# Optimization experiments

Measured on AMD Instinct MI355X. Metric: run time of the kernel, lower is better.

The kernel has to match this reference:

```python
import jax, jax.numpy as jnp
import numpy as np
import math

DIM_IN, DIM_CTX, DIM_KEY, DIM_VAL = 2048, 512, 128, 128
N, T, H, W = 8, 16, 32, 32
NBOX = 512


def setup_inputs() -> dict:
    key = jax.random.key(0)
    ks = jax.random.split(key, 10)
    rois = jax.random.normal(ks[0], (NBOX, DIM_IN), dtype=jnp.float32)
    context = jax.random.normal(ks[1], (N, DIM_CTX, T, H, W), dtype=jnp.float32)
    batch_idx = jnp.sort(jax.random.randint(ks[2], (NBOX,), 0, N))
    s = 0.02
    W_proj = jax.random.normal(ks[3], (DIM_KEY, DIM_IN), dtype=jnp.float32) * s
    b_proj = jnp.zeros((DIM_KEY,), dtype=jnp.float32)
    W_keys = jax.random.normal(ks[4], (DIM_KEY, DIM_CTX), dtype=jnp.float32) * s
    b_keys = jnp.zeros((DIM_KEY,), dtype=jnp.float32)
    W_vals = jax.random.normal(ks[5], (DIM_VAL, DIM_CTX), dtype=jnp.float32) * s
    b_vals = jnp.zeros((DIM_VAL,), dtype=jnp.float32)
    return {"rois": rois, "context": context, "batch_idx": batch_idx,
            "W_proj": W_proj, "b_proj": b_proj,
            "W_keys": W_keys, "b_keys": b_keys,
            "W_vals": W_vals, "b_vals": b_vals}


def reference(rois, context, batch_idx, W_proj, b_proj, W_keys, b_keys, W_vals, b_vals):
    n, c, t, h, w = context.shape
    s = t * h * w
    dk = W_keys.shape[0]
    # ROI query projection: [Nb, dk]
    q = rois @ W_proj.T + b_proj
    # 1x1x1 Conv3d == per-voxel linear over channels
    ctx_flat = context.reshape(n, c, s)                       # [N, C, S]
    keys = jnp.einsum('kc,ncs->nks', W_keys, ctx_flat) + b_keys[None, :, None]  # [N, dk, S]
    vals = jnp.einsum('vc,ncs->nsv', W_vals, ctx_flat) + b_vals[None, None, :]  # [N, S, dv]
    # Per-box gather of its clip's keys/vals, fused cross-attention
    qk = jnp.einsum('bk,bks->bs', q, keys[batch_idx]) / math.sqrt(dk)  # [Nb, S]
    coeff = jax.nn.softmax(qk, axis=-1)
    ctx_out = jnp.einsum('bs,bsv->bv', coeff, vals[batch_idx])         # [Nb, dv]
    attn = coeff.reshape(-1, t, h, w) * 255.0
    return ctx_out, attn
```

## Files before the change

### kernel.cpp

```cpp
#include <hip/hip_runtime.h>
#include <hip/hip_bf16.h>
#include <math.h>

#define DIM_IN  2048
#define DIM_CTX 512
#define DIM_KEY 128
#define DIM_VAL 128
#define NCLIP   8
#define S_TOT   16384
#define NBOX    512
#define MAXB    96

typedef __attribute__((ext_vector_type(8))) short short8_t;
typedef __attribute__((ext_vector_type(4))) float f32x4;

__device__ inline unsigned short f2bf(float x) {
    union { float f; unsigned int u; } v; v.f = x;
    unsigned int r = v.u + 0x7FFFu + ((v.u >> 16) & 1u);
    return (unsigned short)(r >> 16);
}
__device__ inline float bf2f(unsigned short h) {
    union { unsigned int u; float f; } v; v.u = ((unsigned int)h) << 16;
    return v.f;
}

__global__ __launch_bounds__(256) void k0_init(const int* __restrict__ batch_idx,
                                               int* __restrict__ ranges,
                                               float* __restrict__ cctx) {
    int idx = blockIdx.x * blockDim.x + threadIdx.x;
    for (int i = idx; i < NBOX * DIM_CTX; i += gridDim.x * blockDim.x)
        cctx[i] = 0.0f;
    if (blockIdx.x == 0) {
        __shared__ int s_start[NCLIP], s_end[NCLIP];
        if (threadIdx.x < NCLIP) { s_start[threadIdx.x] = NBOX; s_end[threadIdx.x] = 0; }
        __syncthreads();
        for (int i = threadIdx.x; i < NBOX; i += blockDim.x) {
            int b = batch_idx[i];
            atomicMin(&s_start[b], i);
            atomicMax(&s_end[b], i + 1);
        }
        __syncthreads();
        if (threadIdx.x < NCLIP) {
            ranges[threadIdx.x]         = s_start[threadIdx.x];
            ranges[NCLIP + threadIdx.x] = s_end[threadIdx.x];
        }
    }
}

__global__ __launch_bounds__(128) void k1a_q(const float* __restrict__ rois,
                                             const float* __restrict__ W_proj,
                                             const float* __restrict__ b_proj,
                                             float* __restrict__ q) {
    __shared__ float s_roi[4 * DIM_IN];
    int b0 = blockIdx.x * 4;
    const float4* src = (const float4*)(rois + (size_t)b0 * DIM_IN);
    for (int i = threadIdx.x; i < 4 * DIM_IN / 4; i += blockDim.x)
        ((float4*)s_roi)[i] = src[i];
    __syncthreads();
    int k = threadIdx.x;
    const float4* wrow = (const float4*)(W_proj + (size_t)k * DIM_IN);
    float a0 = 0.f, a1 = 0.f, a2 = 0.f, a3 = 0.f;
    for (int i = 0; i < DIM_IN / 4; ++i) {
        float4 w  = wrow[i];
        float4 r0 = *(const float4*)&s_roi[0 * DIM_IN + i * 4];
        float4 r1 = *(const float4*)&s_roi[1 * DIM_IN + i * 4];
        float4 r2 = *(const float4*)&s_roi[2 * DIM_IN + i * 4];
        float4 r3 = *(const float4*)&s_roi[3 * DIM_IN + i * 4];
        a0 += w.x * r0.x; a0 += w.y * r0.y; a0 += w.z * r0.z; a0 += w.w * r0.w;
        a1 += w.x * r1.x; a1 += w.y * r1.y; a1 += w.z * r1.z; a1 += w.w * r1.w;
        a2 += w.x * r2.x; a2 += w.y * r2.y; a2 += w.z * r2.z; a2 += w.w * r2.w;
        a3 += w.x * r3.x; a3 += w.y * r3.y; a3 += w.z * r3.z; a3 += w.w * r3.w;
    }
    float bp = b_proj[k];
    q[(size_t)(b0 + 0) * DIM_KEY + k] = a0 + bp;
    q[(size_t)(b0 + 1) * DIM_KEY + k] = a1 + bp;
    q[(size_t)(b0 + 2) * DIM_KEY + k] = a2 + bp;
    q[(size_t)(b0 + 3) * DIM_KEY + k] = a3 + bp;
}

__global__ __launch_bounds__(256) void k1b_qw(const float* __restrict__ q,
                                              const float* __restrict__ W_keys,
                                              const float* __restrict__ b_keys,
                                              unsigned short* __restrict__ qW_hi,
                                              unsigned short* __restrict__ qW_lo,
                                              float* __restrict__ qbias) {
    __shared__ float s_q[4 * DIM_KEY];
    __shared__ float red[256];
    int b0 = blockIdx.x * 4;
    for (int i = threadIdx.x; i < 4 * DIM_KEY; i += blockDim.x)
        s_q[i] = q[(size_t)b0 * DIM_KEY + i];
    __syncthreads();
    int c0 = threadIdx.x, c1 = threadIdx.x + 256;
    float a[4][2] = {{0.f,0.f},{0.f,0.f},{0.f,0.f},{0.f,0.f}};
    for (int k = 0; k < DIM_KEY; ++k) {
        float w0 = W_keys[(size_t)k * DIM_CTX + c0];
        float w1 = W_keys[(size_t)k * DIM_CTX + c1];
        float q0 = s_q[0 * DIM_KEY + k], q1 = s_q[1 * DIM_KEY + k];
        float q2 = s_q[2 * DIM_KEY + k], q3 = s_q[3 * DIM_KEY + k];
        a[0][0] += q0 * w0; a[0][1] += q0 * w1;
        a[1][0] += q1 * w0; a[1][1] += q1 * w1;
        a[2][0] += q2 * w0; a[2][1] += q2 * w1;
        a[3][0] += q3 * w0; a[3][1] += q3 * w1;
    }
    #pragma unroll
    for (int j = 0; j < 4; ++j) {
        #pragma unroll
        for (int cc = 0; cc < 2; ++cc) {
            int c = (cc == 0) ? c0 : c1;
            float x = a[j][cc];
            unsigned short h = f2bf(x);
            qW_hi[(size_t)(b0 + j) * DIM_CTX + c] = h;
            qW_lo[(size_t)(b0 + j) * DIM_CTX + c] = f2bf(x - bf2f(h));
        }
    }
    for (int j = 0; j < 4; ++j) {
        float v = 0.f;
        if (threadIdx.x < DIM_KEY) v = s_q[j * DIM_KEY + threadIdx.x] * b_keys[threadIdx.x];
        red[threadIdx.x] = v;
        __syncthreads();
        for (int st = 128; st > 0; st >>= 1) {
            if (threadIdx.x < st) red[threadIdx.x] += red[threadIdx.x + st];
            __syncthreads();
        }
        if (threadIdx.x == 0) qbias[b0 + j] = red[0];
        __syncthreads();
    }
}

__global__ __launch_bounds__(256) void k2_scores(
    const float* __restrict__ ctx, const unsigned short* __restrict__ qW_hi,
    const unsigned short* __restrict__ qW_lo, const float* __restrict__ qbias,
    const int* __restrict__ ranges, float* __restrict__ scores)
{
    int n = blockIdx.y;
    int start = ranges[n], Mb = ranges[NCLIP + n] - start;
    if (Mb <= 0) return;
    const float* ctxn = ctx + (size_t)n * DIM_CTX * S_TOT;
    int sch = blockIdx.x * 128;
    int t = threadIdx.x, lane = t & 63, w = t >> 6;

    __shared__ float          ls_f[32 * 132];
    __shared__ unsigned short ls_qh[MAXB * 32];
    __shared__ unsigned short ls_ql[MAXB * 32];
    __shared__ unsigned short ls_th[128 * 32];

    for (int bp = 0; bp < Mb; bp += MAXB) {
        int nb = min(MAXB, Mb - bp);
        f32x4 acc[6][2];
        #pragma unroll
        for (int m = 0; m < 6; ++m)
            #pragma unroll
            for (int nn = 0; nn < 2; ++nn)
                acc[m][nn] = (f32x4){0.f, 0.f, 0.f, 0.f};

        for (int ch = 0; ch < 16; ++ch) {
            int c0 = ch * 32;
            __syncthreads();
            #pragma unroll
            for (int rep = 0; rep < 4; ++rep) {
                int idx = t + rep * 256;
                int c_l = idx >> 5, s4 = (idx & 31) * 4;
                float4 v = *(const float4*)(ctxn + (size_t)(c0 + c_l) * S_TOT + sch + s4);
                *(float4*)&ls_f[c_l * 132 + s4] = v;
            }
            for (int idx = t; idx < MAXB * 4; idx += 256) {
                int row = idx >> 2, c8 = (idx & 3) * 8;
                uint4 vh = {0,0,0,0}, vl = {0,0,0,0};
                if (row < nb) {
                    size_t go = (size_t)(start + bp + row) * DIM_CTX + c0 + c8;
                    vh = *(const uint4*)(qW_hi + go);
                    vl = *(const uint4*)(qW_lo + go);
                }
                int off = (row * 64 + c8 * 2) ^ ((row & 7) << 4);
                *(uint4*)((char*)ls_qh + off) = vh;
                *(uint4*)((char*)ls_ql + off) = vl;
            }
            __syncthreads();
            {
                int s_l = t >> 1, c16 = (t & 1) * 16;
                unsigned short hb[16];
                #pragma unroll
                for (int i = 0; i < 16; ++i)
                    hb[i] = f2bf(ls_f[(c16 + i) * 132 + s_l]);
                int base = s_l * 64 + c16 * 2;
                int sw = (s_l & 7) << 4;
                uint4 p0, p1;
                p0.x = hb[0] | ((unsigned)hb[1] << 16);  p0.y = hb[2] | ((unsigned)hb[3] << 16);
                p0.z = hb[4] | ((unsigned)hb[5] << 16);  p0.w = hb[6] | ((unsigned)hb[7] << 16);
                p1.x = hb[8] | ((unsigned)hb[9] << 16);  p1.y = hb[10] | ((unsigned)hb[11] << 16);
                p1.z = hb[12] | ((unsigned)hb[13] << 16); p1.w = hb[14] | ((unsigned)hb[15] << 16);
                *(uint4*)((char*)ls_th + ((base)      ^ sw)) = p0;
                *(uint4*)((char*)ls_th + ((base + 16) ^ sw)) = p1;
            }
            __syncthreads();
            short8_t Ah[6], Al[6], Bh[2];
            int hi16 = (lane >> 4) * 16;
            #pragma unroll
            for (int m = 0; m < 6; ++m) {
                if (m * 16 < nb) {
                    int row = m * 16 + (lane & 15);
                    int off = (row * 64 + hi16) ^ ((row & 7) << 4);
                    Ah[m] = *(const short8_t*)((const char*)ls_qh + off);
                    Al[m] = *(const short8_t*)((const char*)ls_ql + off);
                }
            }
            #pragma unroll
            for (int nn = 0; nn < 2; ++nn) {
                int srow = (w * 2 + nn) * 16 + (lane & 15);
                int off = (srow * 64 + hi16) ^ ((srow & 7) << 4);
                Bh[nn] = *(const short8_t*)((const char*)ls_th + off);
            }
            #pragma unroll
            for (int m = 0; m < 6; ++m) {
                if (m * 16 < nb) {
                    #pragma unroll
                    for (int nn = 0; nn < 2; ++nn) {
                        acc[m][nn] = __builtin_amdgcn_mfma_f32_16x16x32_bf16(Ah[m], Bh[nn], acc[m][nn], 0, 0, 0);
                        acc[m][nn] = __builtin_amdgcn_mfma_f32_16x16x32_bf16(Al[m], Bh[nn], acc[m][nn], 0, 0, 0);
                    }
                }
            }
        }
        const float rs = 0.08838834764831845f;
        #pragma unroll
        for (int m = 0; m < 6; ++m)
            #pragma unroll
            for (int r = 0; r < 4; ++r) {
                int b_l = m * 16 + ((lane >> 4) << 2) + r;
                if (b_l < nb) {
                    int bg = start + bp + b_l;
                    float qb = qbias[bg];
                    #pragma unroll
                    for (int nn = 0; nn < 2; ++nn) {
                        int s = sch + (w * 2 + nn) * 16 + (lane & 15);
                        scores[(size_t)bg * S_TOT + s] = (acc[m][nn][r] + qb) * rs;
                    }
                }
            }
        __syncthreads();
    }
}

__global__ __launch_bounds__(256) void k3_stats(const float* __restrict__ scores,
                                                float* __restrict__ rmax,
                                                float* __restrict__ rsum) {
    int b = blockIdx.x;
    const float4* row = (const float4*)(scores + (size_t)b * S_TOT);
    __shared__ float red[256];
    float mx = -1e30f;
    for (int i = threadIdx.x; i < S_TOT / 4; i += 256) {
        float4 v = row[i];
        mx = fmaxf(mx, fmaxf(fmaxf(v.x, v.y), fmaxf(v.z, v.w)));
    }
    red[threadIdx.x] = mx;
    __syncthreads();
    for (int st = 128; st > 0; st >>= 1) {
        if (threadIdx.x < st) red[threadIdx.x] = fmaxf(red[threadIdx.x], red[threadIdx.x + st]);
        __syncthreads();
    }
    mx = red[0];
    __syncthreads();
    float sm = 0.f;
    for (int i = threadIdx.x; i < S_TOT / 4; i += 256) {
        float4 v = row[i];
        sm += __expf(v.x - mx) + __expf(v.y - mx) + __expf(v.z - mx) + __expf(v.w - mx);
    }
    red[threadIdx.x] = sm;
    __syncthreads();
    for (int st = 128; st > 0; st >>= 1) {
        if (threadIdx.x < st) red[threadIdx.x] += red[threadIdx.x + st];
        __syncthreads();
    }
    if (threadIdx.x == 0) { rmax[b] = mx; rsum[b] = 1.0f / red[0]; }
}

__global__ __launch_bounds__(256) void k4_pv(
    const float* __restrict__ ctx, const int* __restrict__ ranges,
    const float* __restrict__ rmax, const float* __restrict__ rsum,
    float* __restrict__ attn, float* __restrict__ cctx)
{
    int n = blockIdx.y;
    int start = ranges[n], Mb = ranges[NCLIP + n] - start;
    if (Mb <= 0) return;
    const float* ctxn = ctx + (size_t)n * DIM_CTX * S_TOT;
    int sch = blockIdx.x * 256;
    int t = threadIdx.x, lane = t & 63, w = t >> 6;
    int mh = w >> 1, ns = w & 1;

    __shared__ unsigned short ls_p[MAXB * 256];
    __shared__ unsigned short ls_c[32 * 256];

    for (int bp = 0; bp < Mb; bp += MAXB) {
        int nb = min(MAXB, Mb - bp);
        bool a0v = (mh + 0) * 16 < nb;
        bool a1v = (mh + 2) * 16 < nb;
        bool a2v = (mh + 4) * 16 < nb;
        __syncthreads();
        for (int idx = t; idx < MAXB * 64; idx += 256) {
            int b_l = idx >> 6, s4 = (idx & 63) * 4;
            uint2 pk; pk.x = 0u; pk.y = 0u;
            if (b_l < nb) {
                int bg = start + bp + b_l;
                size_t off = (size_t)bg * S_TOT + sch + s4;
                float4 v = *(const float4*)(attn + off);
                float m = rmax[bg], r = rsum[bg];
                float4 p;
                p.x = __expf(v.x - m) * r; p.y = __expf(v.y - m) * r;
                p.z = __expf(v.z - m) * r; p.w = __expf(v.w - m) * r;
                float4 o;
                o.x = 255.f * p.x; o.y = 255.f * p.y; o.z = 255.f * p.z; o.w = 255.f * p.w;
                *(float4*)(attn + off) = o;
                pk.x = f2bf(p.x) | ((unsigned)f2bf(p.y) << 16);
                pk.y = f2bf(p.z) | ((unsigned)f2bf(p.w) << 16);
            }
            int off8 = (b_l * 512 + s4 * 2) ^ ((b_l & 7) << 4);
            *(uint2*)((char*)ls_p + off8) = pk;
        }
        __syncthreads();
        short8_t A[3][8];
        int hi16 = (lane >> 4) * 16;
        #pragma unroll
        for (int mi = 0; mi < 3; ++mi) {
            int tm = mh + 2 * mi;
            if (tm * 16 < nb) {
                int row = tm * 16 + (lane & 15);
                int sw = (row & 7) << 4;
                #pragma unroll
                for (int k = 0; k < 8; ++k) {
                    int off = (row * 512 + k * 64 + hi16) ^ sw;
                    A[mi][k] = *(const short8_t*)((const char*)ls_p + off);
                }
            }
        }
        for (int ct = 0; ct < 16; ++ct) {
            __syncthreads();
            for (int idx = t; idx < 32 * 64; idx += 256) {
                int c_l = idx >> 6, s4 = (idx & 63) * 4;
                float4 v = *(const float4*)(ctxn + (size_t)(ct * 32 + c_l) * S_TOT + sch + s4);
                uint2 pk;
                pk.x = f2bf(v.x) | ((unsigned)f2bf(v.y) << 16);
                pk.y = f2bf(v.z) | ((unsigned)f2bf(v.w) << 16);
                int off8 = (c_l * 512 + s4 * 2) ^ ((c_l & 7) << 4);
                *(uint2*)((char*)ls_c + off8) = pk;
            }
            __syncthreads();
            f32x4 acc0 = (f32x4){0,0,0,0}, acc1 = (f32x4){0,0,0,0}, acc2 = (f32x4){0,0,0,0};
            int crow = ns * 16 + (lane & 15);
            int swc = (crow & 7) << 4;
            #pragma unroll
            for (int k = 0; k < 8; ++k) {
                int off = (crow * 512 + k * 64 + hi16) ^ swc;
                short8_t B = *(const short8_t*)((const char*)ls_c + off);
                if (a0v) acc0 = __builtin_amdgcn_mfma_f32_16x16x32_bf16(A[0][k], B, acc0, 0, 0, 0);
                if (a1v) acc1 = __builtin_amdgcn_mfma_f32_16x16x32_bf16(A[1][k], B, acc1, 0, 0, 0);
                if (a2v) acc2 = __builtin_amdgcn_mfma_f32_16x16x32_bf16(A[2][k], B, acc2, 0, 0, 0);
            }
            int cg = ct * 32 + ns * 16 + (lane & 15);
            #pragma unroll
            for (int r = 0; r < 4; ++r) {
                int br = ((lane >> 4) << 2) + r;
                int b0l = (mh + 0) * 16 + br;
                int b1l = (mh + 2) * 16 + br;
                int b2l = (mh + 4) * 16 + br;
                if (a0v && b0l < nb) atomicAdd(&cctx[(size_t)(start + bp + b0l) * DIM_CTX + cg], acc0[r]);
                if (a1v && b1l < nb) atomicAdd(&cctx[(size_t)(start + bp + b1l) * DIM_CTX + cg], acc1[r]);
                if (a2v && b2l < nb) atomicAdd(&cctx[(size_t)(start + bp + b2l) * DIM_CTX + cg], acc2[r]);
            }
        }
    }
}

__global__ __launch_bounds__(128) void k5_out(const float* __restrict__ cctx,
                                              const float* __restrict__ W_vals,
                                              const float* __restrict__ b_vals,
                                              float* __restrict__ out) {
    __shared__ float s_c[4 * DIM_CTX];
    int b0 = blockIdx.x * 4;
    const float4* src = (const float4*)(cctx + (size_t)b0 * DIM_CTX);
    for (int i = threadIdx.x; i < 4 * DIM_CTX / 4; i += blockDim.x)
        ((float4*)s_c)[i] = src[i];
    __syncthreads();
    int v = threadIdx.x;
    const float4* wrow = (const float4*)(W_vals + (size_t)v * DIM_CTX);
    float a0 = 0.f, a1 = 0.f, a2 = 0.f, a3 = 0.f;
    for (int i = 0; i < DIM_CTX / 4; ++i) {
        float4 w  = wrow[i];
        float4 c0v = *(const float4*)&s_c[0 * DIM_CTX + i * 4];
        float4 c1v = *(const float4*)&s_c[1 * DIM_CTX + i * 4];
        float4 c2v = *(const float4*)&s_c[2 * DIM_CTX + i * 4];
        float4 c3v = *(const float4*)&s_c[3 * DIM_CTX + i * 4];
        a0 += w.x * c0v.x; a0 += w.y * c0v.y; a0 += w.z * c0v.z; a0 += w.w * c0v.w;
        a1 += w.x * c1v.x; a1 += w.y * c1v.y; a1 += w.z * c1v.z; a1 += w.w * c1v.w;
        a2 += w.x * c2v.x; a2 += w.y * c2v.y; a2 += w.z * c2v.z; a2 += w.w * c2v.w;
        a3 += w.x * c3v.x; a3 += w.y * c3v.y; a3 += w.z * c3v.z; a3 += w.w * c3v.w;
    }
    float bb = b_vals[v];
    out[(size_t)(b0 + 0) * DIM_VAL + v] = a0 + bb;
    out[(size_t)(b0 + 1) * DIM_VAL + v] = a1 + bb;
    out[(size_t)(b0 + 2) * DIM_VAL + v] = a2 + bb;
    out[(size_t)(b0 + 3) * DIM_VAL + v] = a3 + bb;
}

extern "C" void kernel_launch(void* const* d_in, const int* in_sizes, int n_in,
                              void* d_out, int out_size, void* d_ws, size_t ws_size,
                              hipStream_t stream) {
    const float* rois      = (const float*)d_in[0];
    const float* context   = (const float*)d_in[1];
    const int*   batch_idx = (const int*)  d_in[2];
    const float* W_proj    = (const float*)d_in[3];
    const float* b_proj    = (const float*)d_in[4];
    const float* W_keys    = (const float*)d_in[5];
    const float* b_keys    = (const float*)d_in[6];
    const float* W_vals    = (const float*)d_in[7];
    const float* b_vals    = (const float*)d_in[8];

    float* out  = (float*)d_out;
    float* attn = out + NBOX * DIM_VAL;

    char* wsb = (char*)d_ws;
    int*   ranges = (int*)wsb;
    float* q      = (float*)(wsb + 128);
    float* qbias  = q + NBOX * DIM_KEY;
    float* rmaxp  = qbias + NBOX;
    float* rsump  = rmaxp + NBOX;
    float* cctx   = rsump + NBOX;
    unsigned short* qW_hi = (unsigned short*)(cctx + NBOX * DIM_CTX);
    unsigned short* qW_lo = qW_hi + NBOX * DIM_CTX;

    k0_init  <<<dim3(64),       dim3(256), 0, stream>>>(batch_idx, ranges, cctx);
    k1a_q    <<<dim3(NBOX / 4), dim3(128), 0, stream>>>(rois, W_proj, b_proj, q);
    k1b_qw   <<<dim3(NBOX / 4), dim3(256), 0, stream>>>(q, W_keys, b_keys, qW_hi, qW_lo, qbias);
    k2_scores<<<dim3(128, 8),   dim3(256), 0, stream>>>(context, qW_hi, qW_lo, qbias, ranges, attn);
    k3_stats <<<dim3(NBOX),     dim3(256), 0, stream>>>(attn, rmaxp, rsump);
    k4_pv    <<<dim3(64, 8),    dim3(256), 0, stream>>>(context, ranges, rmaxp, rsump, attn, cctx);
    k5_out   <<<dim3(NBOX / 4), dim3(128), 0, stream>>>(cctx, W_vals, b_vals, out);
}
```

Measured before the change: 634.4 us.

## Fuse per-tile softmax max/sum statistics into score kernel epilogue

The score kernel now computes a partial row max and exp-sum for each box over its 128-column tile using shuffles and shared memory, and writes them to a small partial buffer. A tiny reduction kernel merges the 128 partials per box, replacing the stats kernel that re-read the full 512x16384 score matrix twice. This saves a large read pass over the scores in exchange for extra exp and shuffle work in the score epilogue, plus some extra workspace.

```diff
diff --git a/kernel.cpp b/kernel.cpp
--- a/kernel.cpp
+++ b/kernel.cpp
@@ -130,7 +130,8 @@
 __global__ __launch_bounds__(256) void k2_scores(
     const float* __restrict__ ctx, const unsigned short* __restrict__ qW_hi,
     const unsigned short* __restrict__ qW_lo, const float* __restrict__ qbias,
-    const int* __restrict__ ranges, float* __restrict__ scores)
+    const int* __restrict__ ranges, float* __restrict__ scores,
+    float* __restrict__ pmax, float* __restrict__ psum)
 {
     int n = blockIdx.y;
     int start = ranges[n], Mb = ranges[NCLIP + n] - start;
@@ -143,6 +144,8 @@
     __shared__ unsigned short ls_qh[MAXB * 32];
     __shared__ unsigned short ls_ql[MAXB * 32];
     __shared__ unsigned short ls_th[128 * 32];
+    float* red_mx = ls_f;
+    float* red_sm = ls_f + 4 * MAXB;
 
     for (int bp = 0; bp < Mb; bp += MAXB) {
         int nb = min(MAXB, Mb - bp);
@@ -223,55 +226,68 @@
         }
         const float rs = 0.08838834764831845f;
         #pragma unroll
-        for (int m = 0; m < 6; ++m)
+        for (int m = 0; m < 6; ++m) {
+            if (m * 16 >= nb) continue;
             #pragma unroll
             for (int r = 0; r < 4; ++r) {
                 int b_l = m * 16 + ((lane >> 4) << 2) + r;
-                if (b_l < nb) {
-                    int bg = start + bp + b_l;
+                bool valid = b_l < nb;
+                int bg = start + bp + b_l;
+                float sc0, sc1;
+                if (valid) {
                     float qb = qbias[bg];
-                    #pragma unroll
-                    for (int nn = 0; nn < 2; ++nn) {
-                        int s = sch + (w * 2 + nn) * 16 + (lane & 15);
-                        scores[(size_t)bg * S_TOT + s] = (acc[m][nn][r] + qb) * rs;
-                    }
+                    sc0 = (acc[m][0][r] + qb) * rs;
+                    sc1 = (acc[m][1][r] + qb) * rs;
+                    int s0 = sch + (w * 2) * 16 + (lane & 15);
+                    scores[(size_t)bg * S_TOT + s0]      = sc0;
+                    scores[(size_t)bg * S_TOT + s0 + 16] = sc1;
+                } else {
+                    sc0 = sc1 = -1e30f;
                 }
-            }
-        __syncthreads();
-    }
-}
-
-__global__ __launch_bounds__(256) void k3_stats(const float* __restrict__ scores,
-                                                float* __restrict__ rmax,
-                                                float* __restrict__ rsum) {
-    int b = blockIdx.x;
-    const float4* row = (const float4*)(scores + (size_t)b * S_TOT);
-    __shared__ float red[256];
-    float mx = -1e30f;
-    for (int i = threadIdx.x; i < S_TOT / 4; i += 256) {
-        float4 v = row[i];
-        mx = fmaxf(mx, fmaxf(fmaxf(v.x, v.y), fmaxf(v.z, v.w)));
-    }
-    red[threadIdx.x] = mx;
+                float mx = fmaxf(sc0, sc1);
+                #pragma unroll
+                for (int d = 1; d < 16; d <<= 1) mx = fmaxf(mx, __shfl_xor(mx, d, 16));
+                float e = __expf(sc0 - mx) + __expf(sc1 - mx);
+                #pragma unroll
+                for (int d = 1; d < 16; d <<= 1) e += __shfl_xor(e, d, 16);
+                if ((lane & 15) == 0) { red_mx[w * MAXB + b_l] = mx; red_sm[w * MAXB + b_l] = e; }
+            }
+        }
+        __syncthreads();
+        if (t < nb) {
+            float m0 = red_mx[0 * MAXB + t], m1 = red_mx[1 * MAXB + t];
+            float m2 = red_mx[2 * MAXB + t], m3 = red_mx[3 * MAXB + t];
+            float M = fmaxf(fmaxf(m0, m1), fmaxf(m2, m3));
+            float S = red_sm[0 * MAXB + t] * __expf(m0 - M) + red_sm[1 * MAXB + t] * __expf(m1 - M)
+                    + red_sm[2 * MAXB + t] * __expf(m2 - M) + red_sm[3 * MAXB + t] * __expf(m3 - M);
+            int bg = start + bp + t;
+            pmax[(size_t)bg * 128 + blockIdx.x] = M;
+            psum[(size_t)bg * 128 + blockIdx.x] = S;
+        }
+        __syncthreads();
+    }
+}
+
+__global__ __launch_bounds__(128) void k3r(const float* __restrict__ pmax,
+                                           const float* __restrict__ psum,
+                                           float* __restrict__ rmax,
+                                           float* __restrict__ rsum) {
+    int b = blockIdx.x, t = threadIdx.x;
+    float m = pmax[(size_t)b * 128 + t];
+    float s = psum[(size_t)b * 128 + t];
+    __shared__ float sm[2], ss[2];
+    float M = m;
+    #pragma unroll
+    for (int d = 1; d < 64; d <<= 1) M = fmaxf(M, __shfl_xor(M, d, 64));
+    if ((t & 63) == 0) sm[t >> 6] = M;
     __syncthreads();
-    for (int st = 128; st > 0; st >>= 1) {
-        if (threadIdx.x < st) red[threadIdx.x] = fmaxf(red[threadIdx.x], red[threadIdx.x + st]);
-        __syncthreads();
-    }
-    mx = red[0];
+    float Mg = fmaxf(sm[0], sm[1]);
+    float e = s * __expf(m - Mg);
+    #pragma unroll
+    for (int d = 1; d < 64; d <<= 1) e += __shfl_xor(e, d, 64);
+    if ((t & 63) == 0) ss[t >> 6] = e;
     __syncthreads();
-    float sm = 0.f;
-    for (int i = threadIdx.x; i < S_TOT / 4; i += 256) {
-        float4 v = row[i];
-        sm += __expf(v.x - mx) + __expf(v.y - mx) + __expf(v.z - mx) + __expf(v.w - mx);
-    }
-    red[threadIdx.x] = sm;
-    __syncthreads();
-    for (int st = 128; st > 0; st >>= 1) {
-        if (threadIdx.x < st) red[threadIdx.x] += red[threadIdx.x + st];
-        __syncthreads();
-    }
-    if (threadIdx.x == 0) { rmax[b] = mx; rsum[b] = 1.0f / red[0]; }
+    if (t == 0) { rmax[b] = Mg; rsum[b] = 1.0f / (ss[0] + ss[1]); }
 }
 
 __global__ __launch_bounds__(256) void k4_pv(
@@ -424,14 +440,16 @@
     float* rmaxp  = qbias + NBOX;
     float* rsump  = rmaxp + NBOX;
     float* cctx   = rsump + NBOX;
-    unsigned short* qW_hi = (unsigned short*)(cctx + NBOX * DIM_CTX);
+    float* pmaxp  = cctx + NBOX * DIM_CTX;
+    float* psump  = pmaxp + NBOX * 128;
+    unsigned short* qW_hi = (unsigned short*)(psump + NBOX * 128);
     unsigned short* qW_lo = qW_hi + NBOX * DIM_CTX;
 
     k0_init  <<<dim3(64),       dim3(256), 0, stream>>>(batch_idx, ranges, cctx);
     k1a_q    <<<dim3(NBOX / 4), dim3(128), 0, stream>>>(rois, W_proj, b_proj, q);
     k1b_qw   <<<dim3(NBOX / 4), dim3(256), 0, stream>>>(q, W_keys, b_keys, qW_hi, qW_lo, qbias);
-    k2_scores<<<dim3(128, 8),   dim3(256), 0, stream>>>(context, qW_hi, qW_lo, qbias, ranges, attn);
-    k3_stats <<<dim3(NBOX),     dim3(256), 0, stream>>>(attn, rmaxp, rsump);
+    k2_scores<<<dim3(128, 8),   dim3(256), 0, stream>>>(context, qW_hi, qW_lo, qbias, ranges, attn, pmaxp, psump);
+    k3r      <<<dim3(NBOX),     dim3(128), 0, stream>>>(pmaxp, psump, rmaxp, rsump);
     k4_pv    <<<dim3(64, 8),    dim3(256), 0, stream>>>(context, ranges, rmaxp, rsump, attn, cctx);
     k5_out   <<<dim3(NBOX / 4), dim3(128), 0, stream>>>(cctx, W_vals, b_vals, out);
 }
```

After: 639.8 us. Within noise of the previous version (+0.8%).
